# Kernel optimization log

Measured on AMD Instinct MI355X. Metric: run time of the kernel, lower is better.

The kernel has to match this reference:

```python
import jax, jax.numpy as jnp
import numpy as np

D_MODEL = 512
HEADS = 8
D_FF = 1024
EPS = 1e-5


def layer_norm(x, gamma, beta):
    mu = jnp.mean(x, axis=-1, keepdims=True)
    var = jnp.mean(jnp.square(x - mu), axis=-1, keepdims=True)
    return (x - mu) * jax.lax.rsqrt(var + EPS) * gamma + beta


def mha(q, k, v, mask=None):
    # q,k,v: [B, S, D]; no input/output projections in the original module
    B, Sq, D = q.shape
    Sk = k.shape[1]
    dk = D // HEADS
    qh = q.reshape(B, Sq, HEADS, dk).transpose(0, 2, 1, 3)  # [B,H,Sq,dk]
    kh = k.reshape(B, Sk, HEADS, dk).transpose(0, 2, 1, 3)
    vh = v.reshape(B, Sk, HEADS, dk).transpose(0, 2, 1, 3)
    scores = jnp.einsum('bhqd,bhkd->bhqk', qh, kh) / np.sqrt(dk).astype(q.dtype)
    if mask is not None:
        scores = jnp.where(mask == 0, jnp.asarray(-1e9, scores.dtype), scores)
    attn = jax.nn.softmax(scores, axis=-1)  # dropout is identity in eval mode
    out = jnp.einsum('bhqk,bhkd->bhqd', attn, vh)
    return out.transpose(0, 2, 1, 3).reshape(B, Sq, D)


def setup_inputs() -> dict:
    key = jax.random.key(0)
    ks = jax.random.split(key, 8)
    B, S = 4, 2048
    x = jax.random.normal(ks[0], (B, S, D_MODEL), dtype=jnp.float32)
    encoder_output = jax.random.normal(ks[1], (B, S, D_MODEL), dtype=jnp.float32)
    mask = jax.random.randint(ks[2], (B, 1, S, S), 0, 2, dtype=jnp.int32)
    params = {
        'ln1_g': jnp.ones((D_MODEL,), jnp.float32), 'ln1_b': jnp.zeros((D_MODEL,), jnp.float32),
        'ln2_g': jnp.ones((D_MODEL,), jnp.float32), 'ln2_b': jnp.zeros((D_MODEL,), jnp.float32),
        'ln3_g': jnp.ones((D_MODEL,), jnp.float32), 'ln3_b': jnp.zeros((D_MODEL,), jnp.float32),
        'W1': jax.random.normal(ks[3], (D_MODEL, D_FF), jnp.float32) * (1.0 / np.sqrt(D_MODEL)),
        'b1': jnp.zeros((D_FF,), jnp.float32),
        'W2': jax.random.normal(ks[4], (D_FF, D_MODEL), jnp.float32) * (1.0 / np.sqrt(D_FF)),
        'b2': jnp.zeros((D_MODEL,), jnp.float32),
    }
    return {'x': x, 'encoder_output': encoder_output, 'mask': mask, **params}


def reference(x, encoder_output, mask, ln1_g, ln1_b, ln2_g, ln2_b, ln3_g, ln3_b, W1, b1, W2, b2):
    # pre-norm masked self-attention + residual (dropout = identity, eval mode)
    x1 = layer_norm(x, ln1_g, ln1_b)
    x = x + mha(x1, x1, x1, mask)
    # pre-norm cross-attention + residual
    x1 = layer_norm(x, ln2_g, ln2_b)
    x = x + mha(x1, encoder_output, encoder_output, None)
    # pre-norm FFN + residual
    x1 = layer_norm(x, ln3_g, ln3_b)
    h = jax.nn.relu(x1 @ W1 + b1)
    x = x + (h @ W2 + b2)
    return x
```

## Files before the change

kernel.cpp:

```cpp
#include <hip/hip_runtime.h>
#include <hip/hip_bf16.h>

#define D_MODEL 512
#define HEADS   8
#define DK      64
#define D_FF    1024
#define SEQ     2048
#define BATCH   4
#define NTOK    (BATCH*SEQ)
#define NELEM   (NTOK*D_MODEL)

#define QSCALE  0.18033688011112042f
#define MFIX    40.0f

typedef __attribute__((ext_vector_type(8))) short bf8_t;
typedef __attribute__((ext_vector_type(4))) float f4_t;

#define GLD16(gp, lp) __builtin_amdgcn_global_load_lds( \
    (const __attribute__((address_space(1))) void*)(gp), \
    (__attribute__((address_space(3))) void*)(lp), 16, 0, 0)

__device__ __forceinline__ float ldf(const void* p, size_t i, int f32) {
    return f32 ? ((const float*)p)[i] : __bfloat162float(((const __hip_bfloat16*)p)[i]);
}
__device__ __forceinline__ short f2bf(float f) {
    union { __hip_bfloat16 h; short s; } u; u.h = __float2bfloat16(f); return u.s;
}
__device__ __forceinline__ float bf2f(short s) {
    return __uint_as_float(((unsigned)(unsigned short)s) << 16);
}
__device__ __forceinline__ unsigned fbits(float f) { return __float_as_uint(f); }

__global__ void detect_k(const uint4* __restrict__ w, int* __restrict__ flags) {
    __shared__ int found;
    if (threadIdx.x == 0) found = 0;
    __syncthreads();
    int hit = 0;
    for (int i = threadIdx.x; i < 4096; i += 256) {
        uint4 u = w[i];
        if (((u.x & 0x7F80u) == 0x7F80u) || ((u.y & 0x7F80u) == 0x7F80u) ||
            ((u.z & 0x7F80u) == 0x7F80u) || ((u.w & 0x7F80u) == 0x7F80u)) hit = 1;
    }
    if (hit) atomicOr(&found, 1);
    __syncthreads();
    if (threadIdx.x == 0) flags[0] = found ? 1 : 0;
}

__device__ __forceinline__ void transpose_body(const void* src, __hip_bfloat16* dst,
                                               int K, int N, int bxi, int byi, int f32,
                                               __hip_bfloat16 (*t)[33]) {
    int bx = bxi * 32, by = byi * 32;
    int tx = threadIdx.x & 31, ty = threadIdx.x >> 5;
    #pragma unroll
    for (int j = 0; j < 32; j += 8)
        t[ty + j][tx] = __float2bfloat16(ldf(src, (size_t)(by + ty + j) * N + bx + tx, f32));
    __syncthreads();
    #pragma unroll
    for (int j = 0; j < 32; j += 8)
        dst[(size_t)(bx + ty + j) * K + by + tx] = t[tx][ty + j];
}

__global__ __launch_bounds__(256)
void prep_k(const void* __restrict__ enc, const int* __restrict__ mask,
            const void* __restrict__ W1, const void* __restrict__ W2,
            const int* __restrict__ flagp,
            __hip_bfloat16* __restrict__ bufE, unsigned* __restrict__ mb,
            __hip_bfloat16* __restrict__ W1T, __hip_bfloat16* __restrict__ W2T) {
    __shared__ __hip_bfloat16 t[32][33];
    int f32 = *flagp;
    int bid = blockIdx.x;
    if (bid < 16384) {
        int i = bid * 256 + threadIdx.x;
        bufE[i] = __float2bfloat16(ldf(enc, i, f32));
    } else if (bid < 18432) {
        int row  = (bid - 16384) * 4 + (threadIdx.x >> 6);
        int lane = threadIdx.x & 63;
        const int* mr = mask + (size_t)row * SEQ;
        for (int it = 0; it < SEQ/64; it++) {
            unsigned long long bal = __ballot(mr[it*64 + lane] != 0);
            if (lane == 0)  mb[(size_t)row*(SEQ/32) + it*2]     = (unsigned)bal;
            if (lane == 32) mb[(size_t)row*(SEQ/32) + it*2 + 1] = (unsigned)(bal >> 32);
        }
    } else if (bid < 18944) {
        int lb = bid - 18432;
        transpose_body(W1, W1T, D_MODEL, D_FF, lb & 31, lb >> 5, f32, t);
    } else {
        int lb = bid - 18944;
        transpose_body(W2, W2T, D_FF, D_MODEL, lb & 15, lb >> 4, f32, t);
    }
}

__global__ __launch_bounds__(256)
void ln_first_k(const void* __restrict__ x, const void* __restrict__ g,
                const void* __restrict__ b, const int* __restrict__ flagp,
                float* __restrict__ xout, __hip_bfloat16* __restrict__ y) {
    int f32  = *flagp;
    int row  = blockIdx.x * 4 + (threadIdx.x >> 6);
    int lane = threadIdx.x & 63;
    size_t base = (size_t)row * D_MODEL;
    float v[8];
    float s = 0.f;
    #pragma unroll
    for (int i = 0; i < 8; i++) { v[i] = ldf(x, base + lane + i*64, f32); s += v[i]; }
    #pragma unroll
    for (int off = 32; off; off >>= 1) s += __shfl_xor(s, off);
    float mu = s * (1.f / D_MODEL);
    float ss = 0.f;
    #pragma unroll
    for (int i = 0; i < 8; i++) { float d = v[i] - mu; ss += d * d; }
    #pragma unroll
    for (int off = 32; off; off >>= 1) ss += __shfl_xor(ss, off);
    float rstd = rsqrtf(ss * (1.f / D_MODEL) + 1e-5f);
    #pragma unroll
    for (int i = 0; i < 8; i++) {
        int c = lane + i*64;
        xout[base + c] = v[i];
        y[base + c] = __float2bfloat16((v[i] - mu) * rstd * ldf(g, c, f32) + ldf(b, c, f32));
    }
}

__global__ __launch_bounds__(256)
void layernorm_k(const float* __restrict__ x, const void* __restrict__ g,
                 const void* __restrict__ b, const int* __restrict__ flagp,
                 __hip_bfloat16* __restrict__ y) {
    int f32  = *flagp;
    int row  = blockIdx.x * 4 + (threadIdx.x >> 6);
    int lane = threadIdx.x & 63;
    const float* xr = x + (size_t)row * D_MODEL;
    float v[8];
    float s = 0.f;
    #pragma unroll
    for (int i = 0; i < 8; i++) { v[i] = xr[lane + i*64]; s += v[i]; }
    #pragma unroll
    for (int off = 32; off; off >>= 1) s += __shfl_xor(s, off);
    float mu = s * (1.f / D_MODEL);
    float ss = 0.f;
    #pragma unroll
    for (int i = 0; i < 8; i++) { float d = v[i] - mu; ss += d * d; }
    #pragma unroll
    for (int off = 32; off; off >>= 1) ss += __shfl_xor(ss, off);
    float rstd = rsqrtf(ss * (1.f / D_MODEL) + 1e-5f);
    __hip_bfloat16* yr = y + (size_t)row * D_MODEL;
    #pragma unroll
    for (int i = 0; i < 8; i++) {
        int c = lane + i*64;
        yr[c] = __float2bfloat16((v[i] - mu) * rstd * ldf(g, c, f32) + ldf(b, c, f32));
    }
}

__device__ __forceinline__ bf8_t prescale_q(bf8_t q) {
    bf8_t r;
    #pragma unroll
    for (int j = 0; j < 8; j++) r[j] = f2bf(bf2f(q[j]) * QSCALE);
    return r;
}

template<bool HAS_MASK>
__global__ __launch_bounds__(256, 2)
void attn_mfma_k(const __hip_bfloat16* __restrict__ Q, const __hip_bfloat16* __restrict__ K,
                 const __hip_bfloat16* __restrict__ V, const unsigned* __restrict__ mbits,
                 float* __restrict__ Xout) {
    int bid = blockIdx.x;
    int qt = bid & 15;
    int h  = (bid >> 4) & 7;
    int b  = bid >> 7;
    int q0 = qt * 128;
    int tid  = threadIdx.x;
    int w    = tid >> 6;
    int lane = tid & 63;
    int c    = lane & 15;
    int quad = lane >> 4;

    __shared__ __hip_bfloat16 Kt[2][64 * 64];
    __shared__ __hip_bfloat16 VT[2][64 * 64];
    __shared__ __hip_bfloat16 Pb[4][2][16 * 64];

    bf8_t qf[2][2];
    #pragma unroll
    for (int g = 0; g < 2; g++) {
        const __hip_bfloat16* qrp = Q + ((size_t)(b*SEQ + q0 + 32*w + 16*g + c)) * D_MODEL + h*DK;
        qf[g][0] = prescale_q(*(const bf8_t*)(qrp + quad*8));
        qf[g][1] = prescale_q(*(const bf8_t*)(qrp + 32 + quad*8));
    }

    int kpo[4][2], vpo[4][2];
    #pragma unroll
    for (int t = 0; t < 4; t++)
        #pragma unroll
        for (int kh = 0; kh < 2; kh++) {
            int row = 16*t + c;
            kpo[t][kh] = (row*64 + (((4*kh + quad) ^ (row & 7)) * 8)) * 2;
            vpo[t][kh] = (row*64 + (((4*kh + quad) ^ (row & 7) ^ ((row >> 3) & 7)) * 8)) * 2;
        }

    int key0 = (tid >> 3) * 2, d0 = (tid & 7) * 8;
    int vtwo[8];
    #pragma unroll
    for (int j = 0; j < 8; j++) {
        int dk = d0 + j;
        int ch = (key0 >> 3) ^ (dk & 7) ^ ((dk >> 3) & 7);
        vtwo[j] = dk*128 + ch*16 + (key0 & 7)*2;
    }

    int krow[2], kc8[2];
    #pragma unroll
    for (int i = 0; i < 2; i++) {
        int idx = i*256 + tid;
        krow[i] = idx >> 3;
        kc8[i]  = ((idx & 7) ^ (krow[i] & 7)) * 8;
    }

    char* pbw[2] = { (char*)&Pb[w][0][0], (char*)&Pb[w][1][0] };
    int pwoff[4], proff[2];
    #pragma unroll
    for (int nt = 0; nt < 4; nt++)
        pwoff[nt] = c*128 + (((2*nt + (quad >> 1)) ^ (c & 7)) * 16) + (quad & 1)*8;
    #pragma unroll
    for (int kh = 0; kh < 2; kh++)
        proff[kh] = c*128 + (((4*kh + quad) ^ (c & 7)) * 16);

    const unsigned* mrp[2] = {nullptr, nullptr};
    if (HAS_MASK) {
        mrp[0] = mbits + (size_t)(b*SEQ + q0 + 32*w + c) * (SEQ/32);
        mrp[1] = mrp[0] + (size_t)16 * (SEQ/32);
    }
    int qsh = quad * 4;

    short onev = (c == 0) ? (short)0x3F80 : (short)0;
    bf8_t ones = {onev, onev, onev, onev, onev, onev, onev, onev};

    f4_t o[2][4];
    #pragma unroll
    for (int g = 0; g < 2; g++)
        #pragma unroll
        for (int mt = 0; mt < 4; mt++) o[g][mt] = (f4_t){0.f,0.f,0.f,0.f};
    f4_t l_acc[2] = {(f4_t){0.f,0.f,0.f,0.f}, (f4_t){0.f,0.f,0.f,0.f}};

    const size_t kvbase = (size_t)b * SEQ * D_MODEL + (size_t)h * DK;

    for (int ph = 0; ph < SEQ/128; ph++) {
        int k0 = ph * 128;
        __syncthreads();
        #pragma unroll
        for (int t = 0; t < 2; t++) {
            const __hip_bfloat16* Kg = K + kvbase + (size_t)(k0 + t*64) * D_MODEL;
            GLD16(Kg + (size_t)krow[0]*D_MODEL + kc8[0], (char*)&Kt[t][0] + (w*64) * 16);
            GLD16(Kg + (size_t)krow[1]*D_MODEL + kc8[1], (char*)&Kt[t][0] + (256 + w*64) * 16);
        }
        #pragma unroll
        for (int t = 0; t < 2; t++) {
            const __hip_bfloat16* Vg = V + kvbase + (size_t)(k0 + t*64 + key0) * D_MODEL + d0;
            bf8_t v0 = *(const bf8_t*)Vg;
            bf8_t v1 = *(const bf8_t*)(Vg + D_MODEL);
            const unsigned* v0u = (const unsigned*)&v0;
            const unsigned* v1u = (const unsigned*)&v1;
            char* vb = (char*)&VT[t][0];
            #pragma unroll
            for (int dw = 0; dw < 4; dw++) {
                *(unsigned*)(vb + vtwo[2*dw])     = __builtin_amdgcn_perm(v1u[dw], v0u[dw], 0x05040100u);
                *(unsigned*)(vb + vtwo[2*dw + 1]) = __builtin_amdgcn_perm(v1u[dw], v0u[dw], 0x07060302u);
            }
        }
        __syncthreads();

        #pragma unroll
        for (int t = 0; t < 2; t++) {
            const char* ktb = (const char*)&Kt[t][0];
            const char* vtb = (const char*)&VT[t][0];

            f4_t s[2][4];
            #pragma unroll
            for (int nt = 0; nt < 4; nt++) { s[0][nt] = (f4_t){0.f,0.f,0.f,0.f}; s[1][nt] = (f4_t){0.f,0.f,0.f,0.f}; }
            #pragma unroll
            for (int nt = 0; nt < 4; nt++)
                #pragma unroll
                for (int kh = 0; kh < 2; kh++) {
                    bf8_t kf = *(const bf8_t*)(ktb + kpo[nt][kh]);
                    s[0][nt] = __builtin_amdgcn_mfma_f32_16x16x32_bf16(kf, qf[0][kh], s[0][nt], 0, 0, 0);
                    s[1][nt] = __builtin_amdgcn_mfma_f32_16x16x32_bf16(kf, qf[1][kh], s[1][nt], 0, 0, 0);
                }

            #pragma unroll
            for (int g = 0; g < 2; g++) {
                unsigned wq0 = 0xffffffffu, wq1 = 0xffffffffu;
                if (HAS_MASK) {
                    uint2 mw = *(const uint2*)(mrp[g] + ((k0 + t*64) >> 5));
                    wq0 = mw.x >> qsh; wq1 = mw.y >> qsh;
                }
                #pragma unroll
                for (int nt = 0; nt < 4; nt++) {
                    #pragma unroll
                    for (int r = 0; r < 4; r++) {
                        float p = exp2f(s[g][nt][r] - MFIX);
                        if (HAS_MASK) {
                            unsigned sel = (nt < 2) ? wq0 : wq1;
                            if (!((sel >> ((nt & 1)*16 + r)) & 1u)) p = 0.f;
                        }
                        s[g][nt][r] = p;
                    }
                    unsigned pk0 = __builtin_amdgcn_perm(fbits(s[g][nt][1]), fbits(s[g][nt][0]), 0x07060302u);
                    unsigned pk1 = __builtin_amdgcn_perm(fbits(s[g][nt][3]), fbits(s[g][nt][2]), 0x07060302u);
                    *(uint2*)(pbw[g] + pwoff[nt]) = make_uint2(pk0, pk1);
                }
            }

            #pragma unroll
            for (int kh = 0; kh < 2; kh++) {
                bf8_t pfA = *(const bf8_t*)(pbw[0] + proff[kh]);
                bf8_t pfB = *(const bf8_t*)(pbw[1] + proff[kh]);
                l_acc[0] = __builtin_amdgcn_mfma_f32_16x16x32_bf16(ones, pfA, l_acc[0], 0, 0, 0);
                l_acc[1] = __builtin_amdgcn_mfma_f32_16x16x32_bf16(ones, pfB, l_acc[1], 0, 0, 0);
                #pragma unroll
                for (int mt = 0; mt < 4; mt++) {
                    bf8_t vf = *(const bf8_t*)(vtb + vpo[mt][kh]);
                    o[0][mt] = __builtin_amdgcn_mfma_f32_16x16x32_bf16(vf, pfA, o[0][mt], 0, 0, 0);
                    o[1][mt] = __builtin_amdgcn_mfma_f32_16x16x32_bf16(vf, pfB, o[1][mt], 0, 0, 0);
                }
            }
        }
    }

    #pragma unroll
    for (int g = 0; g < 2; g++) {
        float lq = __shfl(l_acc[g][0], c);
        float il = 1.f / fmaxf(lq, 1e-35f);
        size_t rb = ((size_t)(b*SEQ + q0 + 32*w + 16*g + c)) * D_MODEL + h*DK;
        #pragma unroll
        for (int mt = 0; mt < 4; mt++)
            #pragma unroll
            for (int r = 0; r < 4; r++)
                Xout[rb + 16*mt + quad*4 + r] += o[g][mt][r] * il;
    }
}

__global__ __launch_bounds__(256, 2)
void gemm_relu_k(const __hip_bfloat16* __restrict__ A, const __hip_bfloat16* __restrict__ BT,
                 const void* __restrict__ bias, const int* __restrict__ flagp,
                 __hip_bfloat16* __restrict__ C, int Ksz, int Nsz) {
    int f32 = *flagp;
    __shared__ __hip_bfloat16 As[128 * 64];
    __shared__ __hip_bfloat16 Bs[128 * 64];
    int tid  = threadIdx.x;
    int w    = tid >> 6;
    int c    = tid & 15;
    int quad = (tid >> 4) & 3;
    int wy = w >> 1, wx = w & 1;
    int r0 = blockIdx.y * 128, c0 = blockIdx.x * 128;

    f4_t acc[4][4];
    #pragma unroll
    for (int i = 0; i < 4; i++)
        #pragma unroll
        for (int j = 0; j < 4; j++) acc[i][j] = (f4_t){0.f,0.f,0.f,0.f};

    for (int k0 = 0; k0 < Ksz; k0 += 64) {
        __syncthreads();
        #pragma unroll
        for (int i = 0; i < 4; i++) {
            int idx = i*256 + tid;
            int row = idx >> 3, c8 = idx & 7;
            GLD16(A  + (size_t)(r0 + row) * Ksz + k0 + ((c8 ^ (row & 7)) * 8),
                  (char*)As + (size_t)(i*256 + w*64) * 16);
            GLD16(BT + (size_t)(c0 + row) * Ksz + k0 + ((c8 ^ (row & 7)) * 8),
                  (char*)Bs + (size_t)(i*256 + w*64) * 16);
        }
        __syncthreads();

        #pragma unroll
        for (int kh = 0; kh < 2; kh++) {
            bf8_t af[4], bf[4];
            #pragma unroll
            for (int mt = 0; mt < 4; mt++) {
                int row = wy*64 + mt*16 + c;
                af[mt] = *(const bf8_t*)&As[row*64 + (((kh*4 + quad) ^ (row & 7)) * 8)];
            }
            #pragma unroll
            for (int nt = 0; nt < 4; nt++) {
                int row = wx*64 + nt*16 + c;
                bf[nt] = *(const bf8_t*)&Bs[row*64 + (((kh*4 + quad) ^ (row & 7)) * 8)];
            }
            #pragma unroll
            for (int mt = 0; mt < 4; mt++)
                #pragma unroll
                for (int nt = 0; nt < 4; nt++)
                    acc[mt][nt] = __builtin_amdgcn_mfma_f32_16x16x32_bf16(af[mt], bf[nt], acc[mt][nt], 0, 0, 0);
        }
    }

    #pragma unroll
    for (int mt = 0; mt < 4; mt++)
        #pragma unroll
        for (int nt = 0; nt < 4; nt++) {
            int col = c0 + wx*64 + nt*16 + c;
            float bv = ldf(bias, col, f32);
            #pragma unroll
            for (int r = 0; r < 4; r++) {
                int m = r0 + wy*64 + mt*16 + quad*4 + r;
                C[(size_t)m * Nsz + col] = __float2bfloat16(fmaxf(acc[mt][nt][r] + bv, 0.f));
            }
        }
}

__global__ __launch_bounds__(256, 2)
void gemm_out_k(const __hip_bfloat16* __restrict__ A, const __hip_bfloat16* __restrict__ BT,
                const void* __restrict__ bias, const float* __restrict__ resid,
                const int* __restrict__ flagp, void* __restrict__ out, int Ksz, int Nsz) {
    int f32 = *flagp;
    __shared__ __hip_bfloat16 As[128 * 64];
    __shared__ __hip_bfloat16 Bs[64 * 64];
    int tid  = threadIdx.x;
    int w    = tid >> 6;
    int c    = tid & 15;
    int quad = (tid >> 4) & 3;
    int r0 = blockIdx.y * 128, c0 = blockIdx.x * 64;

    f4_t acc[2][4];
    #pragma unroll
    for (int i = 0; i < 2; i++)
        #pragma unroll
        for (int j = 0; j < 4; j++) acc[i][j] = (f4_t){0.f,0.f,0.f,0.f};

    for (int k0 = 0; k0 < Ksz; k0 += 64) {
        __syncthreads();
        #pragma unroll
        for (int i = 0; i < 4; i++) {
            int idx = i*256 + tid;
            int row = idx >> 3, c8 = idx & 7;
            GLD16(A + (size_t)(r0 + row) * Ksz + k0 + ((c8 ^ (row & 7)) * 8),
                  (char*)As + (size_t)(i*256 + w*64) * 16);
        }
        #pragma unroll
        for (int i = 0; i < 2; i++) {
            int idx = i*256 + tid;
            int row = idx >> 3, c8 = idx & 7;
            GLD16(BT + (size_t)(c0 + row) * Ksz + k0 + ((c8 ^ (row & 7)) * 8),
                  (char*)Bs + (size_t)(i*256 + w*64) * 16);
        }
        __syncthreads();

        #pragma unroll
        for (int kh = 0; kh < 2; kh++) {
            bf8_t af[2], bf[4];
            #pragma unroll
            for (int mt = 0; mt < 2; mt++) {
                int row = w*32 + mt*16 + c;
                af[mt] = *(const bf8_t*)&As[row*64 + (((kh*4 + quad) ^ (row & 7)) * 8)];
            }
            #pragma unroll
            for (int nt = 0; nt < 4; nt++) {
                int row = nt*16 + c;
                bf[nt] = *(const bf8_t*)&Bs[row*64 + (((kh*4 + quad) ^ (row & 7)) * 8)];
            }
            #pragma unroll
            for (int mt = 0; mt < 2; mt++)
                #pragma unroll
                for (int nt = 0; nt < 4; nt++)
                    acc[mt][nt] = __builtin_amdgcn_mfma_f32_16x16x32_bf16(af[mt], bf[nt], acc[mt][nt], 0, 0, 0);
        }
    }

    #pragma unroll
    for (int mt = 0; mt < 2; mt++)
        #pragma unroll
        for (int nt = 0; nt < 4; nt++) {
            int col = c0 + nt*16 + c;
            float bv = ldf(bias, col, f32);
            #pragma unroll
            for (int r = 0; r < 4; r++) {
                int m = r0 + w*32 + mt*16 + quad*4 + r;
                float v = acc[mt][nt][r] + bv + resid[(size_t)m * Nsz + col];
                if (f32) ((float*)out)[(size_t)m * Nsz + col] = v;
                else     ((__hip_bfloat16*)out)[(size_t)m * Nsz + col] = __float2bfloat16(v);
            }
        }
}

extern "C" void kernel_launch(void* const* d_in, const int* in_sizes, int n_in,
                              void* d_out, int out_size, void* d_ws, size_t ws_size,
                              hipStream_t stream) {
    const void* x    = d_in[0];
    const void* enc  = d_in[1];
    const int*  mask = (const int*)d_in[2];
    const void* ln1g = d_in[3];
    const void* ln1b = d_in[4];
    const void* ln2g = d_in[5];
    const void* ln2b = d_in[6];
    const void* ln3g = d_in[7];
    const void* ln3b = d_in[8];
    const void* W1   = d_in[9];
    const void* b1   = d_in[10];
    const void* W2   = d_in[11];
    const void* b2   = d_in[12];

    char* ws = (char*)d_ws;
    float*          bufX  = (float*)ws;
    __hip_bfloat16* bufQ  = (__hip_bfloat16*)(ws + (16u<<20));
    __hip_bfloat16* bufE  = (__hip_bfloat16*)(ws + (24u<<20));
    __hip_bfloat16* bufH  = (__hip_bfloat16*)(ws + (32u<<20));
    __hip_bfloat16* W1T   = (__hip_bfloat16*)(ws + (48u<<20));
    __hip_bfloat16* W2T   = (__hip_bfloat16*)(ws + (49u<<20));
    unsigned*       mbits = (unsigned*)(ws + (50u<<20));
    int*            flags = (int*)(ws + (52u<<20));

    dim3 blk(256);
    detect_k<<<1, blk, 0, stream>>>((const uint4*)x, flags);
    prep_k<<<19456, blk, 0, stream>>>(enc, mask, W1, W2, flags, bufE, mbits, W1T, W2T);

    ln_first_k<<<NTOK/4, blk, 0, stream>>>(x, ln1g, ln1b, flags, bufX, bufQ);
    attn_mfma_k<true><<<BATCH*HEADS*(SEQ/128), blk, 0, stream>>>(bufQ, bufQ, bufQ, mbits, bufX);
    layernorm_k<<<NTOK/4, blk, 0, stream>>>(bufX, ln2g, ln2b, flags, bufQ);
    attn_mfma_k<false><<<BATCH*HEADS*(SEQ/128), blk, 0, stream>>>(bufQ, bufE, bufE, nullptr, bufX);
    layernorm_k<<<NTOK/4, blk, 0, stream>>>(bufX, ln3g, ln3b, flags, bufQ);
    gemm_relu_k<<<dim3(D_FF/128, NTOK/128), blk, 0, stream>>>(bufQ, W1T, b1, flags, bufH, D_MODEL, D_FF);
    gemm_out_k<<<dim3(D_MODEL/64, NTOK/128), blk, 0, stream>>>(bufH, W2T, b2, bufX, flags, d_out, D_FF, D_MODEL);
}
```

Before: 375.8 us.

## Double-buffer K/V tiles in attention and prefetch mask bits with raw exp

Doubles the K/V shared-memory buffers so the next 128-key tile's K (async global-to-LDS) and V/mask (into registers) are fetched while the current tile is computed. This leaves one barrier per iteration instead of two. The -MFIX offset is folded into the score accumulator's initial value, and exp2f is replaced with raw v_exp_f32. s_setprio is raised around the MFMA sections, and the output residual update becomes a float4 read-modify-write. The cost is double the LDS footprint (which may hurt occupancy at 2 blocks/CU) and more live registers for the prefetched V and mask data.

```diff
diff --git a/kernel.cpp b/kernel.cpp
--- a/kernel.cpp
+++ b/kernel.cpp
@@ -30,6 +30,10 @@
     return __uint_as_float(((unsigned)(unsigned short)s) << 16);
 }
 __device__ __forceinline__ unsigned fbits(float f) { return __float_as_uint(f); }
+
+__device__ __forceinline__ float fast_exp2(float x) {
+    float r; asm("v_exp_f32 %0, %1" : "=v"(r) : "v"(x)); return r;
+}
 
 __global__ void detect_k(const uint4* __restrict__ w, int* __restrict__ flags) {
     __shared__ int found;
@@ -171,8 +175,8 @@
     int c    = lane & 15;
     int quad = lane >> 4;
 
-    __shared__ __hip_bfloat16 Kt[2][64 * 64];
-    __shared__ __hip_bfloat16 VT[2][64 * 64];
+    __shared__ __hip_bfloat16 Kt[4][64 * 64];
+    __shared__ __hip_bfloat16 VT[4][64 * 64];
     __shared__ __hip_bfloat16 Pb[4][2][16 * 64];
 
     bf8_t qf[2][2];
@@ -238,39 +242,72 @@
 
     const size_t kvbase = (size_t)b * SEQ * D_MODEL + (size_t)h * DK;
 
-    for (int ph = 0; ph < SEQ/128; ph++) {
-        int k0 = ph * 128;
-        __syncthreads();
+    auto loadV = [&](int k0, bf8_t (&r0)[2], bf8_t (&r1)[2]) {
+        #pragma unroll
+        for (int t = 0; t < 2; t++) {
+            const __hip_bfloat16* Vg = V + kvbase + (size_t)(k0 + t*64 + key0) * D_MODEL + d0;
+            r0[t] = *(const bf8_t*)Vg;
+            r1[t] = *(const bf8_t*)(Vg + D_MODEL);
+        }
+    };
+    auto stageK = [&](int k0, int bufbase) {
         #pragma unroll
         for (int t = 0; t < 2; t++) {
             const __hip_bfloat16* Kg = K + kvbase + (size_t)(k0 + t*64) * D_MODEL;
-            GLD16(Kg + (size_t)krow[0]*D_MODEL + kc8[0], (char*)&Kt[t][0] + (w*64) * 16);
-            GLD16(Kg + (size_t)krow[1]*D_MODEL + kc8[1], (char*)&Kt[t][0] + (256 + w*64) * 16);
-        }
+            GLD16(Kg + (size_t)krow[0]*D_MODEL + kc8[0], (char*)&Kt[bufbase + t][0] + (w*64) * 16);
+            GLD16(Kg + (size_t)krow[1]*D_MODEL + kc8[1], (char*)&Kt[bufbase + t][0] + (256 + w*64) * 16);
+        }
+    };
+    auto writeV = [&](const bf8_t (&r0)[2], const bf8_t (&r1)[2], int bufbase) {
         #pragma unroll
         for (int t = 0; t < 2; t++) {
-            const __hip_bfloat16* Vg = V + kvbase + (size_t)(k0 + t*64 + key0) * D_MODEL + d0;
-            bf8_t v0 = *(const bf8_t*)Vg;
-            bf8_t v1 = *(const bf8_t*)(Vg + D_MODEL);
-            const unsigned* v0u = (const unsigned*)&v0;
-            const unsigned* v1u = (const unsigned*)&v1;
-            char* vb = (char*)&VT[t][0];
+            const unsigned* v0u = (const unsigned*)&r0[t];
+            const unsigned* v1u = (const unsigned*)&r1[t];
+            char* vb = (char*)&VT[bufbase + t][0];
             #pragma unroll
             for (int dw = 0; dw < 4; dw++) {
                 *(unsigned*)(vb + vtwo[2*dw])     = __builtin_amdgcn_perm(v1u[dw], v0u[dw], 0x05040100u);
                 *(unsigned*)(vb + vtwo[2*dw + 1]) = __builtin_amdgcn_perm(v1u[dw], v0u[dw], 0x07060302u);
             }
         }
-        __syncthreads();
+    };
+
+    uint4 pm[2];
+    if (HAS_MASK) { pm[0] = *(const uint4*)(mrp[0]); pm[1] = *(const uint4*)(mrp[1]); }
+    bf8_t cv0[2], cv1[2];
+    loadV(0, cv0, cv1);
+    stageK(0, 0);
+    writeV(cv0, cv1, 0);
+    __syncthreads();
+
+    for (int ph = 0; ph < SEQ/128; ph++) {
+        int pb = (ph & 1) ? 2 : 0;
+        int nb = pb ^ 2;
+
+        uint4 nm[2];
+        bf8_t nv0[2], nv1[2];
+        if (ph < SEQ/128 - 1) {
+            int kn = (ph + 1) * 128;
+            if (HAS_MASK) {
+                nm[0] = *(const uint4*)(mrp[0] + (kn >> 5));
+                nm[1] = *(const uint4*)(mrp[1] + (kn >> 5));
+            }
+            loadV(kn, nv0, nv1);
+            stageK(kn, nb);
+        }
 
         #pragma unroll
         for (int t = 0; t < 2; t++) {
-            const char* ktb = (const char*)&Kt[t][0];
-            const char* vtb = (const char*)&VT[t][0];
+            const char* ktb = (const char*)&Kt[pb + t][0];
+            const char* vtb = (const char*)&VT[pb + t][0];
 
             f4_t s[2][4];
             #pragma unroll
-            for (int nt = 0; nt < 4; nt++) { s[0][nt] = (f4_t){0.f,0.f,0.f,0.f}; s[1][nt] = (f4_t){0.f,0.f,0.f,0.f}; }
+            for (int nt = 0; nt < 4; nt++) {
+                s[0][nt] = (f4_t){-MFIX,-MFIX,-MFIX,-MFIX};
+                s[1][nt] = (f4_t){-MFIX,-MFIX,-MFIX,-MFIX};
+            }
+            __builtin_amdgcn_s_setprio(1);
             #pragma unroll
             for (int nt = 0; nt < 4; nt++)
                 #pragma unroll
@@ -279,19 +316,20 @@
                     s[0][nt] = __builtin_amdgcn_mfma_f32_16x16x32_bf16(kf, qf[0][kh], s[0][nt], 0, 0, 0);
                     s[1][nt] = __builtin_amdgcn_mfma_f32_16x16x32_bf16(kf, qf[1][kh], s[1][nt], 0, 0, 0);
                 }
+            __builtin_amdgcn_s_setprio(0);
 
             #pragma unroll
             for (int g = 0; g < 2; g++) {
                 unsigned wq0 = 0xffffffffu, wq1 = 0xffffffffu;
                 if (HAS_MASK) {
-                    uint2 mw = *(const uint2*)(mrp[g] + ((k0 + t*64) >> 5));
-                    wq0 = mw.x >> qsh; wq1 = mw.y >> qsh;
+                    wq0 = (t ? pm[g].z : pm[g].x) >> qsh;
+                    wq1 = (t ? pm[g].w : pm[g].y) >> qsh;
                 }
                 #pragma unroll
                 for (int nt = 0; nt < 4; nt++) {
                     #pragma unroll
                     for (int r = 0; r < 4; r++) {
-                        float p = exp2f(s[g][nt][r] - MFIX);
+                        float p = fast_exp2(s[g][nt][r]);
                         if (HAS_MASK) {
                             unsigned sel = (nt < 2) ? wq0 : wq1;
                             if (!((sel >> ((nt & 1)*16 + r)) & 1u)) p = 0.f;
@@ -304,6 +342,7 @@
                 }
             }
 
+            __builtin_amdgcn_s_setprio(1);
             #pragma unroll
             for (int kh = 0; kh < 2; kh++) {
                 bf8_t pfA = *(const bf8_t*)(pbw[0] + proff[kh]);
@@ -317,7 +356,14 @@
                     o[1][mt] = __builtin_amdgcn_mfma_f32_16x16x32_bf16(vf, pfB, o[1][mt], 0, 0, 0);
                 }
             }
-        }
+            __builtin_amdgcn_s_setprio(0);
+        }
+
+        if (ph < SEQ/128 - 1) {
+            writeV(nv0, nv1, nb);
+            if (HAS_MASK) { pm[0] = nm[0]; pm[1] = nm[1]; }
+        }
+        __syncthreads();
     }
 
     #pragma unroll
@@ -326,10 +372,15 @@
         float il = 1.f / fmaxf(lq, 1e-35f);
         size_t rb = ((size_t)(b*SEQ + q0 + 32*w + 16*g + c)) * D_MODEL + h*DK;
         #pragma unroll
-        for (int mt = 0; mt < 4; mt++)
-            #pragma unroll
-            for (int r = 0; r < 4; r++)
-                Xout[rb + 16*mt + quad*4 + r] += o[g][mt][r] * il;
+        for (int mt = 0; mt < 4; mt++) {
+            float4* xp = (float4*)(Xout + rb + 16*mt + quad*4);
+            float4 x4 = *xp;
+            x4.x += o[g][mt][0] * il;
+            x4.y += o[g][mt][1] * il;
+            x4.z += o[g][mt][2] * il;
+            x4.w += o[g][mt][3] * il;
+            *xp = x4;
+        }
     }
 }
 
```

Result: faster. 343.0 us (-8.7%).
